# Performance work log

Hardware: AMD Instinct MI355X
Metric: run time of the kernel (lower is better)

Reference implementation:

```python
import jax, jax.numpy as jnp
import numpy as np

B, L, H, E, D = 2, 2048, 8, 64, 64

def setup_inputs() -> dict:
    key = jax.random.key(0)
    kq, kk, kv, ks = jax.random.split(key, 4)
    return {
        "queries": jax.random.normal(kq, (B, L, H, E), dtype=jnp.float32),
        "keys": jax.random.normal(kk, (B, L, H, E), dtype=jnp.float32),
        "values": jax.random.normal(kv, (B, L, H, D), dtype=jnp.float32),
        "sigma": jax.random.normal(ks, (B, L, H), dtype=jnp.float32),
    }

def reference(queries, keys, values, sigma):
    b, l, h, e = queries.shape
    scale = 1.0 / np.sqrt(e).astype(np.float32)
    # raw attention scores [B,H,L,S]
    scores = jnp.einsum('blhe,bshe->bhls', queries, keys)
    # strict causal mask (mask j > i)
    causal = jnp.triu(jnp.ones((l, l), dtype=bool), k=1)
    scores = jnp.where(causal[None, None], -jnp.inf, scores)
    attn = scale * scores
    # learned Gaussian prior per query-key distance
    sig = jnp.transpose(sigma, (0, 2, 1))            # [B,H,L]
    sig = jax.nn.sigmoid(sig * 5.0) + 1e-5
    sig = jnp.power(3.0, sig) - 1.0                  # in (0, 2)
    sig = sig[..., None]                             # [B,H,L,1] broadcast over window
    idx = jnp.arange(l, dtype=jnp.float32)
    dist = jnp.abs(idx[:, None] - idx[None, :])      # [L,L]
    inv_sqrt_2pi = 1.0 / np.sqrt(2.0 * np.pi).astype(np.float32)
    prior = (inv_sqrt_2pi / sig) * jnp.exp(-(dist[None, None] ** 2) / (2.0 * sig ** 2))  # [B,H,L,L]
    series = jax.nn.softmax(attn, axis=-1)           # [B,H,L,S]
    V = jnp.einsum('bhls,bshd->blhd', series, values)  # [B,L,H,D]
    sigma_out = jnp.broadcast_to(sig, prior.shape)
    return V, series, prior, sigma_out
```

## Files before the change

kernel.cpp:

```cpp
#include <hip/hip_runtime.h>

#define L_ 2048
#define H_ 8

typedef __attribute__((ext_vector_type(8))) short short8;
typedef __attribute__((ext_vector_type(4))) float f32x4;

static constexpr size_t OFF_S = 2097152;
static constexpr size_t OFF_P = OFF_S + 67108864;
static constexpr size_t OFF_G = OFF_P + 67108864;

static constexpr size_t WS_K = 1u << 20;
static constexpr size_t WS_V = WS_K + (4u << 20);

__device__ __forceinline__ unsigned short f2bf(float x) {
    union { float f; unsigned int u; } c; c.f = x;
    unsigned int u = c.u;
    u += 0x7fffu + ((u >> 16) & 1u);
    return (unsigned short)(u >> 16);
}

__device__ __forceinline__ void gld_lds16(const unsigned short* g, unsigned short* l) {
    __builtin_amdgcn_global_load_lds(
        (const __attribute__((address_space(1))) void*)g,
        (__attribute__((address_space(3))) void*)l, 16, 0, 0);
}

__device__ __forceinline__ void st_nt4(float* p, f32x4 v) {
    __builtin_nontemporal_store(v, reinterpret_cast<f32x4*>(p));
}
__device__ __forceinline__ void st_nt1(float* p, float v) {
    __builtin_nontemporal_store(v, p);
}

__global__ __launch_bounds__(256) void prep(
    const float* __restrict__ k, const float* __restrict__ v,
    unsigned short* __restrict__ wsK, unsigned short* __restrict__ wsV)
{
    const int tid = threadIdx.x;
    const int blk = blockIdx.x;
    __shared__ __attribute__((aligned(16))) unsigned short tr[64][72];
    if (blk < 512) {
        const int bh = blk >> 5, t = blk & 31;
        const int b = bh >> 3, h = bh & 7;
        unsigned short* dst = wsK + (size_t)(bh * 32 + t) * 4096;
        #pragma unroll
        for (int p = 0; p < 2; ++p) {
            const int cid = tid + (p << 8);
            const int r = cid >> 3, c = cid & 7;
            const int j = (t << 6) + r;
            const float4* src = reinterpret_cast<const float4*>(
                k + (((size_t)((b * L_ + j) * H_ + h)) << 6) + (c << 3));
            float4 x0 = src[0], x1 = src[1];
            union { short8 s; unsigned short u[8]; } w;
            w.u[0]=f2bf(x0.x); w.u[1]=f2bf(x0.y); w.u[2]=f2bf(x0.z); w.u[3]=f2bf(x0.w);
            w.u[4]=f2bf(x1.x); w.u[5]=f2bf(x1.y); w.u[6]=f2bf(x1.z); w.u[7]=f2bf(x1.w);
            *reinterpret_cast<short8*>(dst + r * 64 + ((c ^ (r & 7)) << 3)) = w.s;
        }
    } else {
        const int vb = blk - 512;
        const int bh = vb >> 5, t = vb & 31;
        const int b = bh >> 3, h = bh & 7;
        const int col4 = (tid & 15) << 2;
        #pragma unroll
        for (int p = 0; p < 4; ++p) {
            const int r = (tid >> 4) + (p << 4);
            const int j = (t << 6) + r;
            float4 x = *reinterpret_cast<const float4*>(
                v + (((size_t)((b * L_ + j) * H_ + h)) << 6) + col4);
            tr[col4 + 0][r] = f2bf(x.x); tr[col4 + 1][r] = f2bf(x.y);
            tr[col4 + 2][r] = f2bf(x.z); tr[col4 + 3][r] = f2bf(x.w);
        }
        __syncthreads();
        unsigned short* dst = wsV + (size_t)(bh * 32 + t) * 4096;
        #pragma unroll
        for (int p = 0; p < 2; ++p) {
            const int cid = tid + (p << 8);
            const int d = cid >> 3, cj = cid & 7;
            short8 s = *reinterpret_cast<const short8*>(&tr[d][cj << 3]);
            *reinterpret_cast<short8*>(dst + d * 64 + ((cj ^ (d & 7)) << 3)) = s;
        }
    }
}

__global__ __launch_bounds__(256, 4) void fused(
    const float* __restrict__ q, const float* __restrict__ sg,
    const unsigned short* __restrict__ wsK, const unsigned short* __restrict__ wsV,
    float* __restrict__ out)
{
    __shared__ __attribute__((aligned(16))) unsigned short Kb[2][4096];
    __shared__ __attribute__((aligned(16))) unsigned short Vb[2][4096];
    __shared__ __attribute__((aligned(16))) unsigned short Pt[32][72];
    __shared__ float l_sums[32];
    __shared__ float sA[32], sC2[32], sS[32];

    const int tid  = threadIdx.x;
    const int wv   = tid >> 6;
    const int lane = tid & 63;
    const int quad = lane >> 4;
    const int l16  = lane & 15;

    const int blk = blockIdx.x;
    const int s   = 63 - (blk >> 4);
    const int bh  = blk & 15;
    const int b   = bh >> 3, h = bh & 7;
    const int i0  = s << 5;

    const int ntiles = (s >> 1) + 1;
    const unsigned short* gK = wsK + ((size_t)bh * 32) * 4096;
    const unsigned short* gV = wsV + ((size_t)bh * 32) * 4096;

    #define STAGE(buf, t) do {                                              \
        const unsigned short* _sk = gK + (size_t)(t) * 4096;                \
        const unsigned short* _sv = gV + (size_t)(t) * 4096;                \
        _Pragma("unroll")                                                   \
        for (int _qq = 0; _qq < 2; ++_qq) {                                 \
            const int _off = (wv << 10) + (_qq << 9);                       \
            gld_lds16(_sk + _off + (lane << 3), &Kb[buf][_off]);            \
            gld_lds16(_sv + _off + (lane << 3), &Vb[buf][_off]);            \
        }                                                                   \
    } while (0)

    STAGE(0, 0);

    if (tid < 32) {
        l_sums[tid] = 0.0f;
        const int i = i0 + tid;
        const float x = sg[(size_t)((b * L_ + i) * H_ + h)];
        const float sgm = 1.0f / (1.0f + __expf(-5.0f * x)) + 1e-5f;
        const float sp  = expm1f(sgm * 1.0986122886681098f);
        sS[tid]  = sp;
        sA[tid]  = 0.3989422804014327f / sp;
        sC2[tid] = 0.5f / (sp * sp);
    }

    short8 a0[2], a1[2];
    #pragma unroll
    for (int qh = 0; qh < 2; ++qh) {
        const float* qr = q + (((size_t)((b * L_ + (i0 + (qh << 4) + l16)) * H_ + h)) << 6);
        const float4* q4 = reinterpret_cast<const float4*>(qr) + quad * 2;
        float4 x0 = q4[0], x1 = q4[1];
        float4 y0 = q4[8], y1 = q4[9];
        union { short8 v8; unsigned short u[8]; } fa, fb;
        fa.u[0]=f2bf(x0.x); fa.u[1]=f2bf(x0.y); fa.u[2]=f2bf(x0.z); fa.u[3]=f2bf(x0.w);
        fa.u[4]=f2bf(x1.x); fa.u[5]=f2bf(x1.y); fa.u[6]=f2bf(x1.z); fa.u[7]=f2bf(x1.w);
        fb.u[0]=f2bf(y0.x); fb.u[1]=f2bf(y0.y); fb.u[2]=f2bf(y0.z); fb.u[3]=f2bf(y0.w);
        fb.u[4]=f2bf(y1.x); fb.u[5]=f2bf(y1.y); fb.u[6]=f2bf(y1.z); fb.u[7]=f2bf(y1.w);
        a0[qh] = fa.v8; a1[qh] = fb.v8;
    }

    f32x4 oacc[2] = {{0.f,0.f,0.f,0.f}, {0.f,0.f,0.f,0.f}};
    float lpart[2][4] = {{0.f,0.f,0.f,0.f}, {0.f,0.f,0.f,0.f}};
    const int r = (wv << 4) + l16;

    for (int t = 0; t < ntiles; ++t) {
        const int p = t & 1;
        __syncthreads();
        if (t + 1 < ntiles) STAGE(1 - p, t + 1);
        short8 b0 = *reinterpret_cast<const short8*>(&Kb[p][r * 64 + ((quad ^ (r & 7)) << 3)]);
        short8 b1 = *reinterpret_cast<const short8*>(&Kb[p][r * 64 + (((quad + 4) ^ (r & 7)) << 3)]);
        const int j = (t << 6) + r;
        #pragma unroll
        for (int qh = 0; qh < 2; ++qh) {
            f32x4 c4 = {0.f, 0.f, 0.f, 0.f};
            c4 = __builtin_amdgcn_mfma_f32_16x16x32_bf16(a0[qh], b0, c4, 0, 0, 0);
            c4 = __builtin_amdgcn_mfma_f32_16x16x32_bf16(a1[qh], b1, c4, 0, 0, 0);
            #pragma unroll
            for (int rr = 0; rr < 4; ++rr) {
                const int i = i0 + (qh << 4) + (quad << 2) + rr;
                float pv = (j <= i) ? __expf(c4[rr] * 0.125f - 8.0f) : 0.0f;
                lpart[qh][rr] += pv;
                Pt[(qh << 4) + (quad << 2) + rr][r] = f2bf(pv);
            }
        }
        __syncthreads();
        short8 vb0 = *reinterpret_cast<const short8*>(&Vb[p][r * 64 + ((quad ^ (r & 7)) << 3)]);
        short8 vb1 = *reinterpret_cast<const short8*>(&Vb[p][r * 64 + (((quad + 4) ^ (r & 7)) << 3)]);
        #pragma unroll
        for (int qh = 0; qh < 2; ++qh) {
            short8 pa0 = *reinterpret_cast<const short8*>(&Pt[(qh << 4) + l16][quad << 3]);
            short8 pa1 = *reinterpret_cast<const short8*>(&Pt[(qh << 4) + l16][32 + (quad << 3)]);
            oacc[qh] = __builtin_amdgcn_mfma_f32_16x16x32_bf16(pa0, vb0, oacc[qh], 0, 0, 0);
            oacc[qh] = __builtin_amdgcn_mfma_f32_16x16x32_bf16(pa1, vb1, oacc[qh], 0, 0, 0);
        }
    }
    #undef STAGE

    #pragma unroll
    for (int qh = 0; qh < 2; ++qh)
    #pragma unroll
    for (int rr = 0; rr < 4; ++rr) {
        float x = lpart[qh][rr];
        x += __shfl_xor(x, 1); x += __shfl_xor(x, 2);
        x += __shfl_xor(x, 4); x += __shfl_xor(x, 8);
        if (l16 == 0) atomicAdd(&l_sums[(qh << 4) + (quad << 2) + rr], x);
    }
    __syncthreads();

    float inv[2][4];
    #pragma unroll
    for (int qh = 0; qh < 2; ++qh)
    #pragma unroll
    for (int rr = 0; rr < 4; ++rr) {
        inv[qh][rr] = 1.0f / l_sums[(qh << 4) + (quad << 2) + rr];
        const int i = i0 + (qh << 4) + (quad << 2) + rr;
        st_nt1(out + (((size_t)((b * L_ + i) * H_ + h)) << 6) + (wv << 4) + l16,
               oacc[qh][rr] * inv[qh][rr]);
    }

    float* outS = out + OFF_S;
    float* outP = out + OFF_P;
    float* outG = out + OFF_G;
    float* PsA = reinterpret_cast<float*>(&Kb[0][0]);
    float* PsB = reinterpret_cast<float*>(&Vb[0][0]);

    const int rc0  = (wv << 2) + quad;
    const int colc = l16 << 2;
    float Ac[2], C2c[2], fic[2];
    f32x4 svc[2];
    size_t rowbase[2];
    #pragma unroll
    for (int ps = 0; ps < 2; ++ps) {
        const int row = rc0 + (ps << 4);
        Ac[ps]  = sA[row]; C2c[ps] = sC2[row];
        const float Sv = sS[row];
        svc[ps] = (f32x4){Sv, Sv, Sv, Sv};
        fic[ps] = (float)(i0 + row);
        rowbase[ps] = ((size_t)(bh * L_ + i0 + row)) << 11;
    }

    const int off0 = r * 64 + ((quad ^ (r & 7)) << 3);
    const int off1 = r * 64 + (((quad + 4) ^ (r & 7)) << 3);

    short8 kb0 = *reinterpret_cast<const short8*>(gK + off0);
    short8 kb1 = *reinterpret_cast<const short8*>(gK + off1);
    int t = 0;
    for (; t < ntiles; ++t) {
        short8 kn0 = kb0, kn1 = kb1;
        if (t + 1 < ntiles) {
            const unsigned short* kp = gK + (((size_t)(t + 1)) << 12);
            kn0 = *reinterpret_cast<const short8*>(kp + off0);
            kn1 = *reinterpret_cast<const short8*>(kp + off1);
        }
        float* Ps = (t & 1) ? PsB : PsA;
        const int j = (t << 6) + r;
        #pragma unroll
        for (int qh = 0; qh < 2; ++qh) {
            f32x4 c4 = {0.f, 0.f, 0.f, 0.f};
            c4 = __builtin_amdgcn_mfma_f32_16x16x32_bf16(a0[qh], kb0, c4, 0, 0, 0);
            c4 = __builtin_amdgcn_mfma_f32_16x16x32_bf16(a1[qh], kb1, c4, 0, 0, 0);
            #pragma unroll
            for (int rr = 0; rr < 4; ++rr) {
                const int i = i0 + (qh << 4) + (quad << 2) + rr;
                const float pv = (j <= i) ? __expf(c4[rr] * 0.125f - 8.0f) * inv[qh][rr] : 0.0f;
                Ps[((qh << 4) + (quad << 2) + rr) * 68 + r] = pv;
            }
        }
        asm volatile("s_waitcnt lgkmcnt(0)" ::: "memory");
        __builtin_amdgcn_sched_barrier(0);
        __builtin_amdgcn_s_barrier();
        #pragma unroll
        for (int ps = 0; ps < 2; ++ps) {
            const f32x4 se = *reinterpret_cast<const f32x4*>(&Ps[(rc0 + (ps << 4)) * 68 + colc]);
            const int c = (t << 6) + colc;
            const float d0 = fic[ps] - (float)c;
            const float d1 = d0 - 1.f, d2 = d0 - 2.f, d3 = d0 - 3.f;
            f32x4 pr;
            pr.x = Ac[ps] * __expf(-d0 * d0 * C2c[ps]);
            pr.y = Ac[ps] * __expf(-d1 * d1 * C2c[ps]);
            pr.z = Ac[ps] * __expf(-d2 * d2 * C2c[ps]);
            pr.w = Ac[ps] * __expf(-d3 * d3 * C2c[ps]);
            st_nt4(outS + rowbase[ps] + c, se);
            st_nt4(outP + rowbase[ps] + c, pr);
            st_nt4(outG + rowbase[ps] + c, svc[ps]);
        }
        kb0 = kn0; kb1 = kn1;
    }
    const f32x4 z4 = {0.f, 0.f, 0.f, 0.f};
    for (; t < 32; ++t) {
        #pragma unroll
        for (int ps = 0; ps < 2; ++ps) {
            const int c = (t << 6) + colc;
            const float d0 = fic[ps] - (float)c;
            const float d1 = d0 - 1.f, d2 = d0 - 2.f, d3 = d0 - 3.f;
            f32x4 pr;
            pr.x = Ac[ps] * __expf(-d0 * d0 * C2c[ps]);
            pr.y = Ac[ps] * __expf(-d1 * d1 * C2c[ps]);
            pr.z = Ac[ps] * __expf(-d2 * d2 * C2c[ps]);
            pr.w = Ac[ps] * __expf(-d3 * d3 * C2c[ps]);
            st_nt4(outS + rowbase[ps] + c, z4);
            st_nt4(outP + rowbase[ps] + c, pr);
            st_nt4(outG + rowbase[ps] + c, svc[ps]);
        }
    }
}

extern "C" void kernel_launch(void* const* d_in, const int* in_sizes, int n_in,
                              void* d_out, int out_size, void* d_ws, size_t ws_size,
                              hipStream_t stream) {
    const float* q  = (const float*)d_in[0];
    const float* k  = (const float*)d_in[1];
    const float* v  = (const float*)d_in[2];
    const float* sg = (const float*)d_in[3];
    float* outp = (float*)d_out;
    unsigned short* wsK = (unsigned short*)((char*)d_ws + WS_K);
    unsigned short* wsV = (unsigned short*)((char*)d_ws + WS_V);
    prep<<<dim3(1024), dim3(256), 0, stream>>>(k, v, wsK, wsV);
    fused<<<dim3(1024), dim3(256), 0, stream>>>(q, sg, wsK, wsV, outp);
}
```

Baseline: 852.8 us.

## Restructure output writes into 256-column row chunks with rotated chunk ordering

The series-output phase now processes four key tiles per group and stages them in LDS as 32x256 blocks, so each wave writes 1KB contiguous row segments instead of 256-byte pieces. Prior, sigma and zero-fill writes move to a separate pass where each wave covers whole rows in 256-column chunks. Start offsets are rotated per block, wave and row to spread concurrent stores across memory channels. The cost is an extra barrier per group, loss of the cross-tile K prefetch, and prior/sigma stores no longer interleaved with the MFMA work.

Result: faster. 824.8 us (-3.3%).

```diff
diff --git a/kernel.cpp b/kernel.cpp
--- a/kernel.cpp
+++ b/kernel.cpp
@@ -211,86 +211,92 @@
     float* outS = out + OFF_S;
     float* outP = out + OFF_P;
     float* outG = out + OFF_G;
-    float* PsA = reinterpret_cast<float*>(&Kb[0][0]);
-    float* PsB = reinterpret_cast<float*>(&Vb[0][0]);
-
-    const int rc0  = (wv << 2) + quad;
-    const int colc = l16 << 2;
-    float Ac[2], C2c[2], fic[2];
-    f32x4 svc[2];
-    size_t rowbase[2];
-    #pragma unroll
-    for (int ps = 0; ps < 2; ++ps) {
-        const int row = rc0 + (ps << 4);
-        Ac[ps]  = sA[row]; C2c[ps] = sC2[row];
-        const float Sv = sS[row];
-        svc[ps] = (f32x4){Sv, Sv, Sv, Sv};
-        fic[ps] = (float)(i0 + row);
-        rowbase[ps] = ((size_t)(bh * L_ + i0 + row)) << 11;
-    }
+    float* PsLo = reinterpret_cast<float*>(&Kb[0][0]);
+    float* PsHi = reinterpret_cast<float*>(&Vb[0][0]);
 
     const int off0 = r * 64 + ((quad ^ (r & 7)) << 3);
     const int off1 = r * 64 + (((quad + 4) ^ (r & 7)) << 3);
 
-    short8 kb0 = *reinterpret_cast<const short8*>(gK + off0);
-    short8 kb1 = *reinterpret_cast<const short8*>(gK + off1);
-    int t = 0;
-    for (; t < ntiles; ++t) {
-        short8 kn0 = kb0, kn1 = kb1;
-        if (t + 1 < ntiles) {
-            const unsigned short* kp = gK + (((size_t)(t + 1)) << 12);
-            kn0 = *reinterpret_cast<const short8*>(kp + off0);
-            kn1 = *reinterpret_cast<const short8*>(kp + off1);
-        }
-        float* Ps = (t & 1) ? PsB : PsA;
-        const int j = (t << 6) + r;
-        #pragma unroll
-        for (int qh = 0; qh < 2; ++qh) {
-            f32x4 c4 = {0.f, 0.f, 0.f, 0.f};
-            c4 = __builtin_amdgcn_mfma_f32_16x16x32_bf16(a0[qh], kb0, c4, 0, 0, 0);
-            c4 = __builtin_amdgcn_mfma_f32_16x16x32_bf16(a1[qh], kb1, c4, 0, 0, 0);
-            #pragma unroll
-            for (int rr = 0; rr < 4; ++rr) {
-                const int i = i0 + (qh << 4) + (quad << 2) + rr;
-                const float pv = (j <= i) ? __expf(c4[rr] * 0.125f - 8.0f) * inv[qh][rr] : 0.0f;
-                Ps[((qh << 4) + (quad << 2) + rr) * 68 + r] = pv;
+    const int ngl  = (ntiles + 3) >> 2;
+    const int grot = (bh + 3 * s) % ngl;
+
+    for (int g = 0; g < ngl; ++g) {
+        int gv = g + grot; if (gv >= ngl) gv -= ngl;
+        short8 kf0[4], kf1[4];
+        #pragma unroll
+        for (int tl = 0; tl < 4; ++tl) {
+            const int t = (gv << 2) + tl;
+            if (t < ntiles) {
+                const unsigned short* kp = gK + ((size_t)t << 12);
+                kf0[tl] = *reinterpret_cast<const short8*>(kp + off0);
+                kf1[tl] = *reinterpret_cast<const short8*>(kp + off1);
+            }
+        }
+        #pragma unroll
+        for (int tl = 0; tl < 4; ++tl) {
+            const int t = (gv << 2) + tl;
+            const int j = (t << 6) + r;
+            if (t < ntiles) {
+                #pragma unroll
+                for (int qh = 0; qh < 2; ++qh) {
+                    f32x4 c4 = {0.f, 0.f, 0.f, 0.f};
+                    c4 = __builtin_amdgcn_mfma_f32_16x16x32_bf16(a0[qh], kf0[tl], c4, 0, 0, 0);
+                    c4 = __builtin_amdgcn_mfma_f32_16x16x32_bf16(a1[qh], kf1[tl], c4, 0, 0, 0);
+                    float* Pq = qh ? PsHi : PsLo;
+                    #pragma unroll
+                    for (int rr = 0; rr < 4; ++rr) {
+                        const int i = i0 + (qh << 4) + (quad << 2) + rr;
+                        const float pv = (j <= i) ? __expf(c4[rr] * 0.125f - 8.0f) * inv[qh][rr] : 0.0f;
+                        Pq[(((quad << 2) + rr) << 8) + (tl << 6) + r] = pv;
+                    }
+                }
+            } else {
+                #pragma unroll
+                for (int qh = 0; qh < 2; ++qh) {
+                    float* Pq = qh ? PsHi : PsLo;
+                    #pragma unroll
+                    for (int rr = 0; rr < 4; ++rr)
+                        Pq[(((quad << 2) + rr) << 8) + (tl << 6) + r] = 0.0f;
+                }
             }
         }
         asm volatile("s_waitcnt lgkmcnt(0)" ::: "memory");
         __builtin_amdgcn_sched_barrier(0);
         __builtin_amdgcn_s_barrier();
-        #pragma unroll
-        for (int ps = 0; ps < 2; ++ps) {
-            const f32x4 se = *reinterpret_cast<const f32x4*>(&Ps[(rc0 + (ps << 4)) * 68 + colc]);
-            const int c = (t << 6) + colc;
-            const float d0 = fic[ps] - (float)c;
+        float* Pw = (wv < 2) ? PsLo : PsHi;
+        const int rbase = (wv & 1) << 3;
+        #pragma unroll
+        for (int kk = 0; kk < 8; ++kk) {
+            const int row = (wv << 3) + kk;
+            const f32x4 se = *reinterpret_cast<const f32x4*>(&Pw[((rbase + kk) << 8) + (lane << 2)]);
+            st_nt4(outS + (((size_t)(bh * L_ + i0 + row)) << 11) + (gv << 8) + (lane << 2), se);
+        }
+        __builtin_amdgcn_s_barrier();
+    }
+
+    const f32x4 z4 = {0.f, 0.f, 0.f, 0.f};
+    #pragma unroll 1
+    for (int kk = 0; kk < 8; ++kk) {
+        const int row = (wv << 3) + kk;
+        const float Arow = sA[row], C2r = sC2[row], Sv = sS[row];
+        const f32x4 svr = {Sv, Sv, Sv, Sv};
+        const float fi = (float)(i0 + row);
+        const size_t rb = ((size_t)(bh * L_ + i0 + row)) << 11;
+        const int c0 = (bh + s + wv * 3 + kk) & 7;
+        #pragma unroll 1
+        for (int cc = 0; cc < 8; ++cc) {
+            int ch = cc + c0; if (ch >= 8) ch -= 8;
+            const int c = (ch << 8) + (lane << 2);
+            const float d0 = fi - (float)c;
             const float d1 = d0 - 1.f, d2 = d0 - 2.f, d3 = d0 - 3.f;
             f32x4 pr;
-            pr.x = Ac[ps] * __expf(-d0 * d0 * C2c[ps]);
-            pr.y = Ac[ps] * __expf(-d1 * d1 * C2c[ps]);
-            pr.z = Ac[ps] * __expf(-d2 * d2 * C2c[ps]);
-            pr.w = Ac[ps] * __expf(-d3 * d3 * C2c[ps]);
-            st_nt4(outS + rowbase[ps] + c, se);
-            st_nt4(outP + rowbase[ps] + c, pr);
-            st_nt4(outG + rowbase[ps] + c, svc[ps]);
-        }
-        kb0 = kn0; kb1 = kn1;
-    }
-    const f32x4 z4 = {0.f, 0.f, 0.f, 0.f};
-    for (; t < 32; ++t) {
-        #pragma unroll
-        for (int ps = 0; ps < 2; ++ps) {
-            const int c = (t << 6) + colc;
-            const float d0 = fic[ps] - (float)c;
-            const float d1 = d0 - 1.f, d2 = d0 - 2.f, d3 = d0 - 3.f;
-            f32x4 pr;
-            pr.x = Ac[ps] * __expf(-d0 * d0 * C2c[ps]);
-            pr.y = Ac[ps] * __expf(-d1 * d1 * C2c[ps]);
-            pr.z = Ac[ps] * __expf(-d2 * d2 * C2c[ps]);
-            pr.w = Ac[ps] * __expf(-d3 * d3 * C2c[ps]);
-            st_nt4(outS + rowbase[ps] + c, z4);
-            st_nt4(outP + rowbase[ps] + c, pr);
-            st_nt4(outG + rowbase[ps] + c, svc[ps]);
+            pr.x = Arow * __expf(-d0 * d0 * C2r);
+            pr.y = Arow * __expf(-d1 * d1 * C2r);
+            pr.z = Arow * __expf(-d2 * d2 * C2r);
+            pr.w = Arow * __expf(-d3 * d3 * C2r);
+            st_nt4(outP + rb + c, pr);
+            st_nt4(outG + rb + c, svr);
+            if (ch >= ngl) st_nt4(outS + rb + c, z4);
         }
     }
 }
```
